# Optimization experiments

Hardware: AMD Instinct MI355X
Metric: run time of the kernel (lower is better)

## Reference

```python
import jax, jax.numpy as jnp
import numpy as np

N_HEADS = 16
NEG_INF = -1e9


def _apply_rope(xq, xk, cos, sin):
    # xq, xk: [B, S, H, hd]; cos/sin: [S, hd//2]
    def rot(t):
        B, S, H, hd = t.shape
        t = t.reshape(B, S, H, hd // 2, 2)
        t0, t1 = t[..., 0], t[..., 1]
        c = cos[None, :, None, :]
        s = sin[None, :, None, :]
        o0 = t0 * c - t1 * s
        o1 = t0 * s + t1 * c
        return jnp.stack([o0, o1], axis=-1).reshape(B, S, H, hd)
    return rot(xq), rot(xk)


def setup_inputs() -> dict:
    key = jax.random.key(0)
    ks = jax.random.split(key, 7)
    B, S, D = 2, 2048, 2048
    hd = D // N_HEADS
    return {
        "x": jax.random.normal(ks[0], (B, S, D), dtype=jnp.float32),
        "freqs_cos": jax.random.uniform(ks[1], (S, hd // 2), dtype=jnp.float32),
        "freqs_sin": jax.random.uniform(ks[2], (S, hd // 2), dtype=jnp.float32),
        "wq": jax.random.normal(ks[3], (D, D), dtype=jnp.float32) * 0.02,
        "wk": jax.random.normal(ks[4], (D, D), dtype=jnp.float32) * 0.02,
        "wv": jax.random.normal(ks[5], (D, D), dtype=jnp.float32) * 0.02,
        "wo": jax.random.normal(ks[6], (D, D), dtype=jnp.float32) * 0.02,
    }


def reference(x, freqs_cos, freqs_sin, wq, wk, wv, wo):
    B, S, D = x.shape
    H = N_HEADS
    hd = D // H

    # projections (torch Linear: y = x @ W.T)
    xq = (x @ wq.T).reshape(B, S, H, hd)
    xk = (x @ wk.T).reshape(B, S, H, hd)
    xv = (x @ wv.T).reshape(B, S, H, hd)

    xq, xk = _apply_rope(xq, xk, freqs_cos, freqs_sin)

    # [B, H, S, hd]
    q = xq.transpose(0, 2, 1, 3)
    k = xk.transpose(0, 2, 1, 3)
    v = xv.transpose(0, 2, 1, 3)

    scores = jnp.einsum("bhqd,bhkd->bhqk", q, k) / jnp.sqrt(jnp.float32(hd))
    causal = jnp.triu(jnp.full((S, S), NEG_INF, dtype=scores.dtype), k=1)
    scores = scores + causal[None, None]
    probs = jax.nn.softmax(scores.astype(jnp.float32), axis=-1).astype(q.dtype)

    out = jnp.einsum("bhqk,bhkd->bhqd", probs, v)
    out = out.transpose(0, 2, 1, 3).reshape(B, S, D)
    return out @ wo.T
```

## Files before the change

### kernel.cpp

```cpp
#include <hip/hip_runtime.h>
#include <hip/hip_bf16.h>
#include <math.h>

typedef __attribute__((ext_vector_type(8))) short short8;
typedef __attribute__((ext_vector_type(4))) float f32x4;
typedef unsigned short ushort_t;

__device__ __forceinline__ ushort_t f2bf(float f) {
    union { float f; unsigned u; } v; v.f = f;
    unsigned r = v.u + 0x7FFF + ((v.u >> 16) & 1);
    return (ushort_t)(r >> 16);
}
__device__ __forceinline__ float bf2f(short s) {
    union { unsigned u; float f; } v; v.u = ((unsigned)(ushort_t)s) << 16;
    return v.f;
}

__global__ void cvt_kernel(const float* __restrict__ src, ushort_t* __restrict__ dst, int n8) {
    int i = blockIdx.x * blockDim.x + threadIdx.x;
    int stride = gridDim.x * blockDim.x;
    for (; i < n8; i += stride) {
        const float4* s = reinterpret_cast<const float4*>(src) + (size_t)i * 2;
        float4 a = s[0], b = s[1];
        short8 o;
        o[0] = (short)f2bf(a.x); o[1] = (short)f2bf(a.y);
        o[2] = (short)f2bf(a.z); o[3] = (short)f2bf(a.w);
        o[4] = (short)f2bf(b.x); o[5] = (short)f2bf(b.y);
        o[6] = (short)f2bf(b.z); o[7] = (short)f2bf(b.w);
        reinterpret_cast<short8*>(dst)[i] = o;
    }
}

__global__ void cvtw_kernel(const float* __restrict__ w0, const float* __restrict__ w1,
                            const float* __restrict__ w2, const float* __restrict__ w3,
                            ushort_t* __restrict__ dst, int dd8) {
    int i = blockIdx.x * blockDim.x + threadIdx.x;
    int stride = gridDim.x * blockDim.x;
    const int total = dd8 * 4;
    for (; i < total; i += stride) {
        int which = i / dd8;
        int off = i - which * dd8;
        const float* src = (which == 0) ? w0 : (which == 1) ? w1 : (which == 2) ? w2 : w3;
        const float4* s = reinterpret_cast<const float4*>(src) + (size_t)off * 2;
        float4 a = s[0], b = s[1];
        short8 o;
        o[0] = (short)f2bf(a.x); o[1] = (short)f2bf(a.y);
        o[2] = (short)f2bf(a.z); o[3] = (short)f2bf(a.w);
        o[4] = (short)f2bf(b.x); o[5] = (short)f2bf(b.y);
        o[6] = (short)f2bf(b.z); o[7] = (short)f2bf(b.w);
        reinterpret_cast<short8*>(dst)[i] = o;
    }
}

__global__ __launch_bounds__(512, 2) void gemm256_qkv(const ushort_t* __restrict__ A,
                                                      const ushort_t* __restrict__ Bw,
                                                      ushort_t* __restrict__ Cout,
                                                      int M, int N, int K) {
    extern __shared__ __align__(16) ushort_t lds[];
    ushort_t* As = lds;
    ushort_t* Bs = lds + 32768;
    const int t = threadIdx.x;
    const int wid = t >> 6, lane = t & 63;
    const int wr = wid >> 2, wc = wid & 3;
    const int lr = lane & 15, lg = lane >> 4;

    const int ntc = N >> 8;
    const int nwg = (M >> 8) * ntc;
    const int bid = blockIdx.y * gridDim.x + blockIdx.x;
    const int cpx = nwg >> 3;
    const int swz = (bid & 7) * cpx + (bid >> 3);
    const int m0 = (swz / ntc) * 256, n0 = (swz % ntc) * 256;

    f32x4 acc[8][4] = {};

    const int r0 = t >> 3;
    const int c0 = (t & 7) ^ (r0 & 7);
    const ushort_t* gA = A + (long)(m0 + r0) * K + c0 * 8;
    const ushort_t* gB = Bw + (long)(n0 + r0) * K + c0 * 8;

    int aoffE[2];
    aoffE[0] = lr * 64 + (((0 + lg) ^ (lr & 7)) << 3);
    aoffE[1] = lr * 64 + (((4 + lg) ^ (lr & 7)) << 3);

    const int nt = K >> 6;

#define STAGE_A(X, h) do { const int p_ = (X) & 1;                                             \
    __builtin_amdgcn_global_load_lds((const __attribute__((address_space(1))) unsigned int*)   \
        (gA + (long)((h) * 128) * K + (X) * 64),                                               \
        (__attribute__((address_space(3))) unsigned int*)(As + (p_ * 2 + (h)) * 8192 + t * 8), \
        16, 0, 0);                                                                             \
    __builtin_amdgcn_global_load_lds((const __attribute__((address_space(1))) unsigned int*)   \
        (gA + (long)((h) * 128 + 64) * K + (X) * 64),                                          \
        (__attribute__((address_space(3))) unsigned int*)(As + (p_ * 2 + (h)) * 8192 + 4096 + t * 8), \
        16, 0, 0); } while (0)

#define STAGE_B(X, h) do { const int p_ = (X) & 1;                                             \
    __builtin_amdgcn_global_load_lds((const __attribute__((address_space(1))) unsigned int*)   \
        (gB + (long)((h) * 128) * K + (X) * 64),                                               \
        (__attribute__((address_space(3))) unsigned int*)(Bs + (p_ * 2 + (h)) * 8192 + t * 8), \
        16, 0, 0);                                                                             \
    __builtin_amdgcn_global_load_lds((const __attribute__((address_space(1))) unsigned int*)   \
        (gB + (long)((h) * 128 + 64) * K + (X) * 64),                                          \
        (__attribute__((address_space(3))) unsigned int*)(Bs + (p_ * 2 + (h)) * 8192 + 4096 + t * 8), \
        16, 0, 0); } while (0)

#define MIDSYNC() do {                                             \
    asm volatile("" ::: "memory");                                 \
    __builtin_amdgcn_s_barrier();                                  \
    asm volatile("s_waitcnt lgkmcnt(0)" ::: "memory");             \
    __builtin_amdgcn_sched_barrier(0); } while (0)

#define ENDBAR() do {                                              \
    asm volatile("" ::: "memory");                                 \
    __builtin_amdgcn_s_barrier(); } while (0)

#define MFMA_Q(AROW, BCOL, AR, BR) do {                            \
    __builtin_amdgcn_s_setprio(1);                                 \
    _Pragma("unroll")                                              \
    for (int ks = 0; ks < 2; ++ks)                                 \
        _Pragma("unroll")                                          \
        for (int m = 0; m < 4; ++m)                                \
            _Pragma("unroll")                                      \
            for (int n = 0; n < 2; ++n)                            \
                acc[(AROW) + m][(BCOL) + n] =                      \
                    __builtin_amdgcn_mfma_f32_16x16x32_bf16((AR)[m][ks], (BR)[n][ks], acc[(AROW) + m][(BCOL) + n], 0, 0, 0); \
    __builtin_amdgcn_s_setprio(0); } while (0)

#define KTILE(U, BUF) do {                                                                     \
    const int Asb = ((BUF) * 2 + wr) * 8192;                                                   \
    const int Bcb = ((BUF) * 2 + (wc >> 1)) * 8192 + (wc & 1) * 4096;                          \
                                          \
    _Pragma("unroll")                                                                          \
    for (int m = 0; m < 4; ++m)                                                                \
        _Pragma("unroll")                                                                      \
        for (int ks = 0; ks < 2; ++ks)                                                         \
            ar[m][ks] = *reinterpret_cast<const short8*>(&As[Asb + m * 1024 + aoffE[ks]]);     \
    _Pragma("unroll")                                                                          \
    for (int n = 0; n < 2; ++n)                                                                \
        _Pragma("unroll")                                                                      \
        for (int ks = 0; ks < 2; ++ks)                                                         \
            br0[n][ks] = *reinterpret_cast<const short8*>(&Bs[Bcb + n * 1024 + aoffE[ks]]);    \
    if ((U) + 1 < nt) STAGE_A((U) + 1, 1);                                                     \
    MIDSYNC();                                                                                 \
    MFMA_Q(0, 0, ar, br0);                                                                     \
    ENDBAR();                                                                                  \
                                                                  \
    _Pragma("unroll")                                                                          \
    for (int n = 0; n < 2; ++n)                                                                \
        _Pragma("unroll")                                                                      \
        for (int ks = 0; ks < 2; ++ks)                                                         \
            br1[n][ks] = *reinterpret_cast<const short8*>(&Bs[Bcb + 2048 + n * 1024 + aoffE[ks]]); \
    MIDSYNC();                                                                                 \
    MFMA_Q(0, 2, ar, br1);                                                                     \
    ENDBAR();                                                                                  \
                                                 \
    _Pragma("unroll")                                                                          \
    for (int m = 0; m < 4; ++m)                                                                \
        _Pragma("unroll")                                                                      \
        for (int ks = 0; ks < 2; ++ks)                                                         \
            ar[m][ks] = *reinterpret_cast<const short8*>(&As[Asb + 4096 + m * 1024 + aoffE[ks]]); \
    if ((U) + 2 < nt) STAGE_B((U) + 2, 0);                                                     \
    MIDSYNC();                                                                                 \
    MFMA_Q(4, 2, ar, br1);                                                                     \
    ENDBAR();                                                                                  \
                                  \
    if ((U) + 2 < nt) { STAGE_A((U) + 2, 0); STAGE_B((U) + 2, 1); }                            \
    asm volatile("" ::: "memory");                                                             \
    __builtin_amdgcn_s_barrier();                                                              \
    MFMA_Q(4, 0, ar, br0);                                                                     \
    if ((U) < nt - 2) {                                                                        \
        asm volatile("s_waitcnt vmcnt(6)" ::: "memory");                                       \
    } else if ((U) == nt - 2) {                                                                \
        asm volatile("s_waitcnt vmcnt(0)" ::: "memory");                                       \
    }                                                                                          \
    __builtin_amdgcn_s_barrier(); } while (0)

    STAGE_A(0, 0); STAGE_A(0, 1); STAGE_B(0, 0); STAGE_B(0, 1);
    STAGE_A(1, 0); STAGE_B(1, 0); STAGE_B(1, 1);
    asm volatile("s_waitcnt vmcnt(6)" ::: "memory");
    __builtin_amdgcn_s_barrier();

    short8 ar[4][2], br0[2][2], br1[2][2];

    for (int U = 0; U < nt; U += 2) {
        KTILE(U, 0);
        KTILE(U + 1, 1);
    }
#undef KTILE
#undef MFMA_Q
#undef ENDBAR
#undef MIDSYNC
#undef STAGE_A
#undef STAGE_B

    #pragma unroll
    for (int m = 0; m < 8; ++m) {
        #pragma unroll
        for (int n = 0; n < 4; ++n) {
            const int col = n0 + wc * 64 + n * 16 + lr;
            const int which = col >> 11;
            const int h = (col >> 7) & 15;
            const int d = col & 127;
            #pragma unroll
            for (int r = 0; r < 4; ++r) {
                const int row = m0 + wr * 128 + m * 16 + lg * 4 + r;
                const int bb = row >> 11, s = row & 2047;
                Cout[(long)which * M * 2048 + (((long)(bb * 16 + h)) * 2048 + s) * 128 + d] = f2bf(acc[m][n][r]);
            }
        }
    }
}

template<int OUT_MODE>
__global__ __launch_bounds__(256) void gemm_nt(const ushort_t* __restrict__ A,
                                               const ushort_t* __restrict__ Bw,
                                               void* __restrict__ Cout,
                                               int M, int N, int K) {
    __shared__ __align__(16) ushort_t As[2 * 128 * 32];
    __shared__ __align__(16) ushort_t Bs[2 * 128 * 32];
    const int t = threadIdx.x;
    const int wid = t >> 6, lane = t & 63;
    const int wm = wid >> 1, wn = wid & 1;
    const int lr = lane & 15, lg = lane >> 4;

    const int ntc = N >> 7;
    const int nwg = (M >> 7) * ntc;
    const int bid = blockIdx.y * gridDim.x + blockIdx.x;
    const int cpx = nwg >> 3;
    const int swz = (bid & 7) * cpx + (bid >> 3);
    const int m0 = (swz / ntc) * 128, n0 = (swz % ntc) * 128;

    f32x4 acc[4][4] = {};

    const int sh0 = wid * 1024 + lane * 8;
    const int sh1 = sh0 + 512;
    const int r0 = sh0 >> 5, c0 = sh0 & 31;
    const int r1 = sh1 >> 5, c1 = sh1 & 31;

    const ushort_t* gA0 = A + (long)(m0 + r0) * K + c0;
    const ushort_t* gA1 = A + (long)(m0 + r1) * K + c1;
    const ushort_t* gB0 = Bw + (long)(n0 + r0) * K + c0;
    const ushort_t* gB1 = Bw + (long)(n0 + r1) * K + c1;

    auto stage = [&](int k0, int nb) {
        ushort_t* as = As + nb * 4096;
        ushort_t* bs = Bs + nb * 4096;
        __builtin_amdgcn_global_load_lds((const __attribute__((address_space(1))) unsigned int*)(gA0 + k0),
                                         (__attribute__((address_space(3))) unsigned int*)(as + sh0), 16, 0, 0);
        __builtin_amdgcn_global_load_lds((const __attribute__((address_space(1))) unsigned int*)(gA1 + k0),
                                         (__attribute__((address_space(3))) unsigned int*)(as + sh1), 16, 0, 0);
        __builtin_amdgcn_global_load_lds((const __attribute__((address_space(1))) unsigned int*)(gB0 + k0),
                                         (__attribute__((address_space(3))) unsigned int*)(bs + sh0), 16, 0, 0);
        __builtin_amdgcn_global_load_lds((const __attribute__((address_space(1))) unsigned int*)(gB1 + k0),
                                         (__attribute__((address_space(3))) unsigned int*)(bs + sh1), 16, 0, 0);
    };

    const int nt = K >> 5;
    stage(0, 0);
    __syncthreads();
    int cur = 0;

    for (int ti = 0; ti < nt; ++ti) {
        if (ti + 1 < nt) stage((ti + 1) << 5, cur ^ 1);
        const ushort_t* as = As + cur * 4096;
        const ushort_t* bs = Bs + cur * 4096;
        short8 af[4], bfr[4];
        #pragma unroll
        for (int m = 0; m < 4; ++m)
            af[m] = *reinterpret_cast<const short8*>(&as[(wm * 64 + m * 16 + lr) * 32 + lg * 8]);
        #pragma unroll
        for (int n = 0; n < 4; ++n)
            bfr[n] = *reinterpret_cast<const short8*>(&bs[(wn * 64 + n * 16 + lr) * 32 + lg * 8]);
        #pragma unroll
        for (int m = 0; m < 4; ++m)
            #pragma unroll
            for (int n = 0; n < 4; ++n)
                acc[m][n] = __builtin_amdgcn_mfma_f32_16x16x32_bf16(af[m], bfr[n], acc[m][n], 0, 0, 0);
        __syncthreads();
        cur ^= 1;
    }

    #pragma unroll
    for (int m = 0; m < 4; ++m) {
        #pragma unroll
        for (int n = 0; n < 4; ++n) {
            const int col = n0 + wn * 64 + n * 16 + lr;
            #pragma unroll
            for (int r = 0; r < 4; ++r) {
                const int row = m0 + wm * 64 + m * 16 + lg * 4 + r;
                float v = acc[m][n][r];
                if (OUT_MODE == 0) {
                    ((float*)Cout)[(long)row * N + col] = v;
                } else {
                    const int which = col >> 11;
                    const int h = (col >> 7) & 15;
                    const int d = col & 127;
                    const int b = row >> 11, s = row & 2047;
                    ((ushort_t*)Cout)[(long)which * M * 2048 +
                                      (((long)(b * 16 + h)) * 2048 + s) * 128 + d] = f2bf(v);
                }
            }
        }
    }
}

__global__ void rope_kernel(ushort_t* __restrict__ X, const float* __restrict__ fc,
                            const float* __restrict__ fs, int total8) {
    int i = blockIdx.x * blockDim.x + threadIdx.x;
    if (i >= total8) return;
    const int s_idx = (i >> 4) & 2047;
    const int i0 = (i & 15) * 4;
    const long base = (long)i * 8;
    short8 v = *reinterpret_cast<const short8*>(X + base);
    short8 o;
    #pragma unroll
    for (int p = 0; p < 4; ++p) {
        float c  = fc[(long)s_idx * 64 + i0 + p];
        float sn = fs[(long)s_idx * 64 + i0 + p];
        float x0 = bf2f(v[2 * p]), x1 = bf2f(v[2 * p + 1]);
        o[2 * p]     = (short)f2bf(x0 * c - x1 * sn);
        o[2 * p + 1] = (short)f2bf(x0 * sn + x1 * c);
    }
    *reinterpret_cast<short8*>(X + base) = o;
}

__global__ void vtrans_kernel(const ushort_t* __restrict__ Vp, ushort_t* __restrict__ Vt,
                              int S) {
    const int bh = blockIdx.y;
    const int s0 = blockIdx.x * 16 + ((threadIdx.x >> 7) * 8);
    const int d = threadIdx.x & 127;
    const ushort_t* src = Vp + (long)bh * S * 128;
    short8 o;
    #pragma unroll
    for (int i = 0; i < 8; ++i)
        o[i] = (short)src[(long)(s0 + i) * 128 + d];
    *reinterpret_cast<short8*>(Vt + ((long)bh * 128 + d) * S + s0) = o;
}

__global__ __launch_bounds__(256, 3) void attn_kernel(const ushort_t* __restrict__ Qp,
                                                      const ushort_t* __restrict__ Kp,
                                                      const ushort_t* __restrict__ Vtg,
                                                      ushort_t* __restrict__ O,
                                                      int S, int H) {
    __shared__ __align__(16) ushort_t Ks[64][136];
    __shared__ __align__(16) ushort_t Vs[128][72];
    __shared__ __align__(16) ushort_t Pl[4][16][72];
    const int t = threadIdx.x, wid = t >> 6, lane = t & 63;
    const int lr = lane & 15, lg = lane >> 4;
    const int bh = blockIdx.y;
    const int b = bh / H, h = bh % H;
    const ushort_t* Qh = Qp + (long)bh * S * 128;
    const ushort_t* Kh = Kp + (long)bh * S * 128;
    const ushort_t* Vth = Vtg + (long)bh * 128 * S;
    const int nq = S / 64;
    const float scale = 0.08838834764831845f;

    const int ksr = t >> 2;
    const int ksc = (t & 3) * 32;
    const int vsr = t & 127;
    const int vsc = (t >> 7) * 32;

    for (int qsel = 0; qsel < 2; ++qsel) {
        const int qt = qsel ? (nq - 1 - blockIdx.x) : blockIdx.x;
        const int qb0 = qt * 64;

        const int qrow = qb0 + wid * 16 + lr;
        short8 qf[4];
        #pragma unroll
        for (int kk = 0; kk < 4; ++kk)
            qf[kk] = *reinterpret_cast<const short8*>(Qh + (long)qrow * 128 + kk * 32 + lg * 8);

        f32x4 oacc[8] = {};
        float mrow[4], lsum[4];
        #pragma unroll
        for (int r = 0; r < 4; ++r) { mrow[r] = -INFINITY; lsum[r] = 0.f; }

        const int nkt = qt + 1;

        short8 kreg[4], vreg[4];
        {
            const ushort_t* kgp = Kh + t * 32;
            const ushort_t* vgp = Vth + (long)vsr * S + vsc;
            #pragma unroll
            for (int j = 0; j < 4; ++j) kreg[j] = *reinterpret_cast<const short8*>(kgp + j * 8);
            #pragma unroll
            for (int j = 0; j < 4; ++j) vreg[j] = *reinterpret_cast<const short8*>(vgp + j * 8);
        }

        for (int kt = 0; kt < nkt; ++kt) {
            const int kv0 = kt * 64;
            __syncthreads();
            #pragma unroll
            for (int j = 0; j < 4; ++j)
                *reinterpret_cast<short8*>(&Ks[ksr][ksc + j * 8]) = kreg[j];
            #pragma unroll
            for (int j = 0; j < 4; ++j)
                *reinterpret_cast<short8*>(&Vs[vsr][vsc + j * 8]) = vreg[j];
            __syncthreads();
            if (kt + 1 < nkt) {
                const ushort_t* kgp = Kh + (long)(kv0 + 64) * 128 + t * 32;
                const ushort_t* vgp = Vth + (long)vsr * S + kv0 + 64 + vsc;
                #pragma unroll
                for (int j = 0; j < 4; ++j) kreg[j] = *reinterpret_cast<const short8*>(kgp + j * 8);
                #pragma unroll
                for (int j = 0; j < 4; ++j) vreg[j] = *reinterpret_cast<const short8*>(vgp + j * 8);
            }

            f32x4 sacc[4] = {};
            #pragma unroll
            for (int kk = 0; kk < 4; ++kk) {
                #pragma unroll
                for (int n = 0; n < 4; ++n) {
                    short8 kf = *reinterpret_cast<const short8*>(&Ks[n * 16 + lr][kk * 32 + lg * 8]);
                    sacc[n] = __builtin_amdgcn_mfma_f32_16x16x32_bf16(qf[kk], kf, sacc[n], 0, 0, 0);
                }
            }
            float sv[4][4];
            const int myq = qb0 + wid * 16 + lg * 4;
            #pragma unroll
            for (int n = 0; n < 4; ++n) {
                int kcol = kv0 + n * 16 + lr;
                #pragma unroll
                for (int r = 0; r < 4; ++r) {
                    float xv = sacc[n][r] * scale;
                    sv[n][r] = (kcol > myq + r) ? -1e9f : xv;
                }
            }
            float alpha[4];
            #pragma unroll
            for (int r = 0; r < 4; ++r) {
                float mx = fmaxf(fmaxf(sv[0][r], sv[1][r]), fmaxf(sv[2][r], sv[3][r]));
                #pragma unroll
                for (int off = 1; off < 16; off <<= 1)
                    mx = fmaxf(mx, __shfl_xor(mx, off));
                float mnew = fmaxf(mrow[r], mx);
                alpha[r] = __expf(mrow[r] - mnew);
                float ts = 0.f;
                #pragma unroll
                for (int n = 0; n < 4; ++n) {
                    float p = __expf(sv[n][r] - mnew);
                    sv[n][r] = p;
                    ts += p;
                }
                #pragma unroll
                for (int off = 1; off < 16; off <<= 1)
                    ts += __shfl_xor(ts, off);
                lsum[r] = lsum[r] * alpha[r] + ts;
                mrow[r] = mnew;
            }
            #pragma unroll
            for (int f = 0; f < 8; ++f)
                #pragma unroll
                for (int r = 0; r < 4; ++r)
                    oacc[f][r] *= alpha[r];
            #pragma unroll
            for (int n = 0; n < 4; ++n)
                #pragma unroll
                for (int r = 0; r < 4; ++r)
                    Pl[wid][lg * 4 + r][n * 16 + lr] = f2bf(sv[n][r]);
            __asm volatile("" ::: "memory");
            short8 pf[2];
            #pragma unroll
            for (int ks = 0; ks < 2; ++ks)
                pf[ks] = *reinterpret_cast<const short8*>(&Pl[wid][lr][ks * 32 + lg * 8]);
            #pragma unroll
            for (int ks = 0; ks < 2; ++ks) {
                #pragma unroll
                for (int f = 0; f < 8; ++f) {
                    short8 vf = *reinterpret_cast<const short8*>(&Vs[f * 16 + lr][ks * 32 + lg * 8]);
                    oacc[f] = __builtin_amdgcn_mfma_f32_16x16x32_bf16(pf[ks], vf, oacc[f], 0, 0, 0);
                }
            }
        }
        float inv[4];
        #pragma unroll
        for (int r = 0; r < 4; ++r) inv[r] = 1.f / lsum[r];
        ushort_t* Oh = O + (long)b * S * 2048 + h * 128;
        #pragma unroll
        for (int f = 0; f < 8; ++f) {
            #pragma unroll
            for (int r = 0; r < 4; ++r) {
                int row = qb0 + wid * 16 + lg * 4 + r;
                int col = f * 16 + lr;
                Oh[(long)row * 2048 + col] = f2bf(oacc[f][r] * inv[r]);
            }
        }
    }
}

extern "C" void kernel_launch(void* const* d_in, const int* in_sizes, int n_in,
                              void* d_out, int out_size, void* d_ws, size_t ws_size,
                              hipStream_t stream) {
    const float* x  = (const float*)d_in[0];
    const float* fc = (const float*)d_in[1];
    const float* fs = (const float*)d_in[2];
    const float* wq = (const float*)d_in[3];
    const float* wk = (const float*)d_in[4];
    const float* wv = (const float*)d_in[5];
    const float* wo = (const float*)d_in[6];
    float* out = (float*)d_out;

    const int B = 2, S = 2048, D = 2048, H = 16;
    const int M = B * S;
    const size_t MD = (size_t)M * D;
    const size_t DD = (size_t)D * D;

    char* ws = (char*)d_ws;
    ushort_t* xbf = (ushort_t*)ws;
    ushort_t* wqb = (ushort_t*)(ws + MD * 2);
    ushort_t* wob = wqb + 3 * DD;
    ushort_t* qp  = wqb + 4 * DD;
    ushort_t* kp  = qp + MD;
    ushort_t* vp  = kp + MD;
    ushort_t* vtg   = xbf;
    ushort_t* attnb = vp;

    cvt_kernel<<<2048, 256, 0, stream>>>(x, xbf, (int)(MD / 8));
    cvtw_kernel<<<2048, 256, 0, stream>>>(wq, wk, wv, wo, wqb, (int)(DD / 8));

    dim3 gq(6144 / 256, M / 256);
    gemm256_qkv<<<gq, 512, 131072, stream>>>(xbf, wqb, qp, M, 3 * D, D);

    const int total8 = (int)(2 * MD / 8);
    rope_kernel<<<(total8 + 255) / 256, 256, 0, stream>>>(qp, fc, fs, total8);

    dim3 gv(S / 16, B * H);
    vtrans_kernel<<<gv, 256, 0, stream>>>(vp, vtg, S);
    dim3 ga(S / 128, B * H);
    attn_kernel<<<ga, 256, 0, stream>>>(qp, kp, vtg, attnb, S, H);

    dim3 gg(D / 128, M / 128);
    gemm_nt<0><<<gg, 256, 0, stream>>>(attnb, wob, out, M, D, D);
}
```

Baseline: 322.9 us.

## Fuse RoPE and V transpose into QKV GEMM epilogue, merge conversion kernels

The QKV GEMM epilogue now applies the rotary embedding to Q and K in registers, pairing adjacent columns with a lane shuffle, and writes V directly in transposed layout. This removes the separate rope and vtrans kernels and their extra global read/write passes. The two fp32-to-bf16 conversion kernels are merged into one launch. The epilogue does more work, with cos/sin loads and a shuffle per element, and the V store is a strided 4-element write. Workspace aliasing changes so that the attention output reuses the x buffer.

```diff
diff --git a/kernel.cpp b/kernel.cpp
--- a/kernel.cpp
+++ b/kernel.cpp
@@ -3,6 +3,7 @@
 #include <math.h>
 
 typedef __attribute__((ext_vector_type(8))) short short8;
+typedef __attribute__((ext_vector_type(4))) short short4v;
 typedef __attribute__((ext_vector_type(4))) float f32x4;
 typedef unsigned short ushort_t;
 
@@ -16,11 +17,24 @@
     return v.f;
 }
 
-__global__ void cvt_kernel(const float* __restrict__ src, ushort_t* __restrict__ dst, int n8) {
+__global__ void cvt_all(const float* __restrict__ x,
+                        const float* __restrict__ w0, const float* __restrict__ w1,
+                        const float* __restrict__ w2, const float* __restrict__ w3,
+                        ushort_t* __restrict__ dst, int md8, int dd8) {
     int i = blockIdx.x * blockDim.x + threadIdx.x;
     int stride = gridDim.x * blockDim.x;
-    for (; i < n8; i += stride) {
-        const float4* s = reinterpret_cast<const float4*>(src) + (size_t)i * 2;
+    const int total = md8 + 4 * dd8;
+    for (; i < total; i += stride) {
+        const float* src;
+        long off;
+        if (i < md8) { src = x; off = i; }
+        else {
+            int j = i - md8;
+            int which = j / dd8;
+            off = j - (long)which * dd8;
+            src = (which == 0) ? w0 : (which == 1) ? w1 : (which == 2) ? w2 : w3;
+        }
+        const float4* s = reinterpret_cast<const float4*>(src) + off * 2;
         float4 a = s[0], b = s[1];
         short8 o;
         o[0] = (short)f2bf(a.x); o[1] = (short)f2bf(a.y);
@@ -31,30 +45,12 @@
     }
 }
 
-__global__ void cvtw_kernel(const float* __restrict__ w0, const float* __restrict__ w1,
-                            const float* __restrict__ w2, const float* __restrict__ w3,
-                            ushort_t* __restrict__ dst, int dd8) {
-    int i = blockIdx.x * blockDim.x + threadIdx.x;
-    int stride = gridDim.x * blockDim.x;
-    const int total = dd8 * 4;
-    for (; i < total; i += stride) {
-        int which = i / dd8;
-        int off = i - which * dd8;
-        const float* src = (which == 0) ? w0 : (which == 1) ? w1 : (which == 2) ? w2 : w3;
-        const float4* s = reinterpret_cast<const float4*>(src) + (size_t)off * 2;
-        float4 a = s[0], b = s[1];
-        short8 o;
-        o[0] = (short)f2bf(a.x); o[1] = (short)f2bf(a.y);
-        o[2] = (short)f2bf(a.z); o[3] = (short)f2bf(a.w);
-        o[4] = (short)f2bf(b.x); o[5] = (short)f2bf(b.y);
-        o[6] = (short)f2bf(b.z); o[7] = (short)f2bf(b.w);
-        reinterpret_cast<short8*>(dst)[i] = o;
-    }
-}
-
 __global__ __launch_bounds__(512, 2) void gemm256_qkv(const ushort_t* __restrict__ A,
                                                       const ushort_t* __restrict__ Bw,
                                                       ushort_t* __restrict__ Cout,
+                                                      ushort_t* __restrict__ Vt,
+                                                      const float* __restrict__ fc,
+                                                      const float* __restrict__ fs,
                                                       int M, int N, int K) {
     extern __shared__ __align__(16) ushort_t lds[];
     ushort_t* As = lds;
@@ -129,7 +125,6 @@
 #define KTILE(U, BUF) do {                                                                     \
     const int Asb = ((BUF) * 2 + wr) * 8192;                                                   \
     const int Bcb = ((BUF) * 2 + (wc >> 1)) * 8192 + (wc & 1) * 4096;                          \
-                                          \
     _Pragma("unroll")                                                                          \
     for (int m = 0; m < 4; ++m)                                                                \
         _Pragma("unroll")                                                                      \
@@ -144,7 +139,6 @@
     MIDSYNC();                                                                                 \
     MFMA_Q(0, 0, ar, br0);                                                                     \
     ENDBAR();                                                                                  \
-                                                                  \
     _Pragma("unroll")                                                                          \
     for (int n = 0; n < 2; ++n)                                                                \
         _Pragma("unroll")                                                                      \
@@ -153,7 +147,6 @@
     MIDSYNC();                                                                                 \
     MFMA_Q(0, 2, ar, br1);                                                                     \
     ENDBAR();                                                                                  \
-                                                 \
     _Pragma("unroll")                                                                          \
     for (int m = 0; m < 4; ++m)                                                                \
         _Pragma("unroll")                                                                      \
@@ -163,7 +156,6 @@
     MIDSYNC();                                                                                 \
     MFMA_Q(4, 2, ar, br1);                                                                     \
     ENDBAR();                                                                                  \
-                                  \
     if ((U) + 2 < nt) { STAGE_A((U) + 2, 0); STAGE_B((U) + 2, 1); }                            \
     asm volatile("" ::: "memory");                                                             \
     __builtin_amdgcn_s_barrier();                                                              \
@@ -193,6 +185,7 @@
 #undef STAGE_A
 #undef STAGE_B
 
+    const int S = 2048;
     #pragma unroll
     for (int m = 0; m < 8; ++m) {
         #pragma unroll
@@ -201,21 +194,35 @@
             const int which = col >> 11;
             const int h = (col >> 7) & 15;
             const int d = col & 127;
-            #pragma unroll
-            for (int r = 0; r < 4; ++r) {
-                const int row = m0 + wr * 128 + m * 16 + lg * 4 + r;
-                const int bb = row >> 11, s = row & 2047;
-                Cout[(long)which * M * 2048 + (((long)(bb * 16 + h)) * 2048 + s) * 128 + d] = f2bf(acc[m][n][r]);
-            }
-        }
-    }
-}
-
-template<int OUT_MODE>
-__global__ __launch_bounds__(256) void gemm_nt(const ushort_t* __restrict__ A,
-                                               const ushort_t* __restrict__ Bw,
-                                               void* __restrict__ Cout,
-                                               int M, int N, int K) {
+            const int rowb = m0 + wr * 128 + m * 16 + lg * 4;
+            const int bb = rowb >> 11;
+            const int sb = rowb & 2047;
+            if (which == 2) {
+                short4v o;
+                #pragma unroll
+                for (int r = 0; r < 4; ++r) o[r] = (short)f2bf(acc[m][n][r]);
+                *reinterpret_cast<short4v*>(Vt + ((long)(bb * 16 + h) * 128 + d) * S + sb) = o;
+            } else {
+                const int i0 = d >> 1;
+                #pragma unroll
+                for (int r = 0; r < 4; ++r) {
+                    const int s = sb + r;
+                    float v = acc[m][n][r];
+                    float p = __shfl_xor(v, 1);
+                    float c  = fc[(long)s * 64 + i0];
+                    float sn = fs[(long)s * 64 + i0];
+                    float o = (lr & 1) ? (p * sn + v * c) : (v * c - p * sn);
+                    Cout[(long)which * M * 2048 + (((long)(bb * 16 + h)) * 2048 + s) * 128 + d] = f2bf(o);
+                }
+            }
+        }
+    }
+}
+
+__global__ __launch_bounds__(256) void gemm_nt_f32(const ushort_t* __restrict__ A,
+                                                   const ushort_t* __restrict__ Bw,
+                                                   float* __restrict__ Cout,
+                                                   int M, int N, int K) {
     __shared__ __align__(16) ushort_t As[2 * 128 * 32];
     __shared__ __align__(16) ushort_t Bs[2 * 128 * 32];
     const int t = threadIdx.x;
@@ -288,53 +295,10 @@
             #pragma unroll
             for (int r = 0; r < 4; ++r) {
                 const int row = m0 + wm * 64 + m * 16 + lg * 4 + r;
-                float v = acc[m][n][r];
-                if (OUT_MODE == 0) {
-                    ((float*)Cout)[(long)row * N + col] = v;
-                } else {
-                    const int which = col >> 11;
-                    const int h = (col >> 7) & 15;
-                    const int d = col & 127;
-                    const int b = row >> 11, s = row & 2047;
-                    ((ushort_t*)Cout)[(long)which * M * 2048 +
-                                      (((long)(b * 16 + h)) * 2048 + s) * 128 + d] = f2bf(v);
-                }
-            }
-        }
-    }
-}
-
-__global__ void rope_kernel(ushort_t* __restrict__ X, const float* __restrict__ fc,
-                            const float* __restrict__ fs, int total8) {
-    int i = blockIdx.x * blockDim.x + threadIdx.x;
-    if (i >= total8) return;
-    const int s_idx = (i >> 4) & 2047;
-    const int i0 = (i & 15) * 4;
-    const long base = (long)i * 8;
-    short8 v = *reinterpret_cast<const short8*>(X + base);
-    short8 o;
-    #pragma unroll
-    for (int p = 0; p < 4; ++p) {
-        float c  = fc[(long)s_idx * 64 + i0 + p];
-        float sn = fs[(long)s_idx * 64 + i0 + p];
-        float x0 = bf2f(v[2 * p]), x1 = bf2f(v[2 * p + 1]);
-        o[2 * p]     = (short)f2bf(x0 * c - x1 * sn);
-        o[2 * p + 1] = (short)f2bf(x0 * sn + x1 * c);
-    }
-    *reinterpret_cast<short8*>(X + base) = o;
-}
-
-__global__ void vtrans_kernel(const ushort_t* __restrict__ Vp, ushort_t* __restrict__ Vt,
-                              int S) {
-    const int bh = blockIdx.y;
-    const int s0 = blockIdx.x * 16 + ((threadIdx.x >> 7) * 8);
-    const int d = threadIdx.x & 127;
-    const ushort_t* src = Vp + (long)bh * S * 128;
-    short8 o;
-    #pragma unroll
-    for (int i = 0; i < 8; ++i)
-        o[i] = (short)src[(long)(s0 + i) * 128 + d];
-    *reinterpret_cast<short8*>(Vt + ((long)bh * 128 + d) * S + s0) = o;
+                Cout[(long)row * N + col] = acc[m][n][r];
+            }
+        }
+    }
 }
 
 __global__ __launch_bounds__(256, 3) void attn_kernel(const ushort_t* __restrict__ Qp,
@@ -511,24 +475,17 @@
     ushort_t* wob = wqb + 3 * DD;
     ushort_t* qp  = wqb + 4 * DD;
     ushort_t* kp  = qp + MD;
-    ushort_t* vp  = kp + MD;
-    ushort_t* vtg   = xbf;
-    ushort_t* attnb = vp;
-
-    cvt_kernel<<<2048, 256, 0, stream>>>(x, xbf, (int)(MD / 8));
-    cvtw_kernel<<<2048, 256, 0, stream>>>(wq, wk, wv, wo, wqb, (int)(DD / 8));
+    ushort_t* vtg = kp + MD;
+    ushort_t* attnb = xbf;
+
+    cvt_all<<<2048, 256, 0, stream>>>(x, wq, wk, wv, wo, xbf, (int)(MD / 8), (int)(DD / 8));
 
     dim3 gq(6144 / 256, M / 256);
-    gemm256_qkv<<<gq, 512, 131072, stream>>>(xbf, wqb, qp, M, 3 * D, D);
-
-    const int total8 = (int)(2 * MD / 8);
-    rope_kernel<<<(total8 + 255) / 256, 256, 0, stream>>>(qp, fc, fs, total8);
-
-    dim3 gv(S / 16, B * H);
-    vtrans_kernel<<<gv, 256, 0, stream>>>(vp, vtg, S);
+    gemm256_qkv<<<gq, 512, 131072, stream>>>(xbf, wqb, qp, vtg, fc, fs, M, 3 * D, D);
+
     dim3 ga(S / 128, B * H);
     attn_kernel<<<ga, 256, 0, stream>>>(qp, kp, vtg, attnb, S, H);
 
     dim3 gg(D / 128, M / 128);
-    gemm_nt<0><<<gg, 256, 0, stream>>>(attnb, wob, out, M, D, D);
-}
+    gemm_nt_f32<<<gg, 256, 0, stream>>>(attnb, wob, out, M, D, D);
+}
```

Result: faster. 306.5 us (-5.1%).
